# Kernel optimization log

Hardware: AMD Instinct MI355X
Metric: run time of the kernel (lower is better)

The kernel has to match this reference:

```python
import jax, jax.numpy as jnp
import numpy as np

N_NODES = 100000
N_EDGES = 1600000
N_GRAPHS = 1000


def setup_inputs() -> dict:
    key = jax.random.key(0)
    ks = jax.random.split(key, 20)
    s = 0.1
    inp = {
        'x': jax.random.normal(ks[0], (N_NODES, 7), jnp.float32),
        'edge_attr': jax.random.normal(ks[1], (N_EDGES, 4), jnp.float32),
        # edge linear (edge_dim -> in_channels) per conv
        'W_e1': jax.random.normal(ks[2], (4, 7), jnp.float32) * s,
        'b_e1': jnp.zeros((7,), jnp.float32),
        'W_e2': jax.random.normal(ks[3], (4, 64), jnp.float32) * s,
        'b_e2': jnp.zeros((64,), jnp.float32),
        # conv1 MLP: Linear(7,64) -> ReLU -> Linear(64,64)
        'W1a': jax.random.normal(ks[4], (7, 64), jnp.float32) * s,
        'b1a': jnp.zeros((64,), jnp.float32),
        'W1b': jax.random.normal(ks[5], (64, 64), jnp.float32) * s,
        'b1b': jnp.zeros((64,), jnp.float32),
        # conv2 MLP: Linear(64,64) -> ReLU -> Linear(64,64)
        'W2a': jax.random.normal(ks[6], (64, 64), jnp.float32) * s,
        'b2a': jnp.zeros((64,), jnp.float32),
        'W2b': jax.random.normal(ks[7], (64, 64), jnp.float32) * s,
        'b2b': jnp.zeros((64,), jnp.float32),
        # final classifier Linear(64, 12)
        'Wfc': jax.random.normal(ks[8], (64, 12), jnp.float32) * s,
        'bfc': jnp.zeros((12,), jnp.float32),
        'edge_index': jax.random.randint(ks[9], (2, N_EDGES), 0, N_NODES, jnp.int64),
        'batch': jnp.sort(jax.random.randint(ks[10], (N_NODES,), 0, N_GRAPHS, jnp.int64)),
    }
    return inp


def _gine_conv(x, edge_index, edge_attr, W_e, b_e, Wa, ba, Wb, bb):
    # GINEConv (eps=0): nn(x_i + sum_j relu(x_j + lin_e(e_ji)))
    src, dst = edge_index[0], edge_index[1]
    e = edge_attr @ W_e + b_e                      # [E, d]
    m = jax.nn.relu(x[src] + e)                    # gather + message [E, d]
    agg = jax.ops.segment_sum(m, dst, num_segments=x.shape[0])  # scatter-add
    h = x + agg                                    # (1+eps)*x with eps=0
    return jax.nn.relu(h @ Wa + ba) @ Wb + bb


def reference(x, edge_attr, W_e1, b_e1, W_e2, b_e2, W1a, b1a, W1b, b1b,
              W2a, b2a, W2b, b2b, Wfc, bfc, edge_index, batch):
    h = jax.nn.relu(_gine_conv(x, edge_index, edge_attr, W_e1, b_e1, W1a, b1a, W1b, b1b))
    h = jax.nn.relu(_gine_conv(h, edge_index, edge_attr, W_e2, b_e2, W2a, b2a, W2b, b2b))
    # global mean pool over graphs
    sums = jax.ops.segment_sum(h, batch, num_segments=N_GRAPHS)          # [G, 64]
    cnt = jax.ops.segment_sum(jnp.ones((h.shape[0], 1), h.dtype), batch,
                              num_segments=N_GRAPHS)                      # [G, 1]
    pooled = sums / jnp.maximum(cnt, 1.0)
    return pooled @ Wfc + bfc                                             # [G, 12]
```

## Files before the change

kernel.cpp:

```cpp
#include <hip/hip_runtime.h>
#include <hip/hip_bf16.h>


#define NBUCK 512
#define TILE_A 2048
#define PB_CAP 3584

typedef __attribute__((ext_vector_type(8))) short bf16x8;
typedef __attribute__((ext_vector_type(4))) float f32x4;
typedef __attribute__((ext_vector_type(4))) unsigned int u32x4;

__device__ __forceinline__ float bf2f(unsigned short u) {
  return __uint_as_float(((unsigned)u) << 16);
}
__device__ __forceinline__ unsigned short f2bf(float f) {
  __hip_bfloat16 hb = __float2bfloat16(f);
  return *reinterpret_cast<unsigned short*>(&hb);
}
__device__ __forceinline__ int bucket_lo(int b, int N) {
  return (int)(((long long)b * N + (NBUCK - 1)) >> 9);
}
__device__ __forceinline__ int bucket_of(int d, int N, float f512overN) {
  int b = (int)((float)d * f512overN);
  long long d512 = (long long)d << 9;
  if ((long long)(b + 1) * N <= d512) ++b;
  else if ((long long)b * N > d512) --b;
  return b;
}

__global__ __launch_bounds__(256) void histB_kernel(
    const int* __restrict__ dstIdx, int* __restrict__ bcnt, int E, int N,
    float f512overN) {
  __shared__ int cnt[NBUCK];
  int t = threadIdx.x;
  cnt[t] = 0;
  cnt[t + 256] = 0;
  __syncthreads();
  int e0 = blockIdx.x * TILE_A;
  int valid = min(TILE_A, E - e0);
#pragma unroll
  for (int k = 0; k < 8; ++k) {
    int idx = t + k * 256;
    if (idx < valid) {
      int d = dstIdx[e0 + idx];
      atomicAdd(&cnt[bucket_of(d, N, f512overN)], 1);
    }
  }
  __syncthreads();
  if (cnt[t]) atomicAdd(&bcnt[t], cnt[t]);
  if (cnt[t + 256]) atomicAdd(&bcnt[t + 256], cnt[t + 256]);
}

__global__ __launch_bounds__(256) void scanB_kernel(
    const int* __restrict__ bcnt, int* __restrict__ bstart,
    int* __restrict__ bcur, int E) {
  __shared__ int sd[256];
  int t = threadIdx.x;
  int base = t * 2;
  int v0 = bcnt[base];
  int v1 = bcnt[base + 1];
  int ts = v0 + v1;
  sd[t] = ts;
  __syncthreads();
  for (int off = 1; off < 256; off <<= 1) {
    int xv = (t >= off) ? sd[t - off] : 0;
    __syncthreads();
    sd[t] += xv;
    __syncthreads();
  }
  int excl = sd[t] - ts;
  bstart[base] = excl;
  bstart[base + 1] = excl + v0;
  bcur[base] = excl;
  bcur[base + 1] = excl + v0;
  if (t == 255) bstart[NBUCK] = E;
}

__global__ __launch_bounds__(256) void binA_kernel(
    const int* __restrict__ srcIdx, const int* __restrict__ dstIdx,
    const float* __restrict__ ea, int* __restrict__ bcur,
    u32x4* __restrict__ binned, int E, int N, float f512overN) {
  __shared__ u32x4 recs[TILE_A];
  __shared__ int cnt[NBUCK];
  __shared__ int off[NBUCK];
  int t = threadIdx.x;
  int e0 = blockIdx.x * TILE_A;
  int valid = min(TILE_A, E - e0);

  cnt[t] = 0;
  cnt[t + 256] = 0;
  __syncthreads();

  u32x4 rec[8];
  int bkt[8], slot[8];
#pragma unroll
  for (int k = 0; k < 8; ++k) {
    int idx = t + k * 256;
    bkt[k] = -1;
    if (idx < valid) {
      int e = e0 + idx;
      int d = dstIdx[e];
      int s = __builtin_nontemporal_load(&srcIdx[e]);
      f32x4 a = __builtin_nontemporal_load(
          reinterpret_cast<const f32x4*>(ea) + e);
      u32x4 v;
      v[0] = (unsigned)s;
      v[1] = (unsigned)f2bf(a[0]) | ((unsigned)f2bf(a[1]) << 16);
      v[2] = (unsigned)f2bf(a[2]) | ((unsigned)f2bf(a[3]) << 16);
      v[3] = (unsigned)d;
      rec[k] = v;
      int b = bucket_of(d, N, f512overN);
      bkt[k] = b;
      slot[k] = atomicAdd(&cnt[b], 1);
    }
  }
  __syncthreads();
  int c0 = cnt[t], c1 = cnt[t + 256];
  for (int o = 1; o < NBUCK; o <<= 1) {
    int v0 = (t >= o) ? cnt[t - o] : 0;
    int v1 = (t + 256 >= o) ? cnt[t + 256 - o] : 0;
    __syncthreads();
    cnt[t] += v0;
    cnt[t + 256] += v1;
    __syncthreads();
  }
  off[t] = cnt[t] - c0;
  off[t + 256] = cnt[t + 256] - c1;
  __syncthreads();
#pragma unroll
  for (int k = 0; k < 8; ++k)
    if (bkt[k] >= 0) recs[off[bkt[k]] + slot[k]] = rec[k];
  __syncthreads();
#pragma unroll
  for (int h = 0; h < 2; ++h) {
    int b = t + h * 256;
    int c = (h == 0) ? c0 : c1;
    if (c > 0) {
      int g = atomicAdd(&bcur[b], c);
      int o = off[b];
      for (int k = 0; k < c; ++k) binned[g + k] = recs[o + k];
    }
  }
}

__global__ __launch_bounds__(256) void binB_kernel(
    const u32x4* __restrict__ binned, const int* __restrict__ bstart,
    int* __restrict__ deg, int* __restrict__ cursor, int* __restrict__ gcur,
    u32x4* __restrict__ csr, const float* __restrict__ x,
    const float* __restrict__ We1, const float* __restrict__ be1,
    float* __restrict__ p1, int N) {
  __shared__ u32x4 lrec[PB_CAP];
  __shared__ int ldeg[256];
  __shared__ int lcur[256];
  int b = blockIdx.x;
  int t = threadIdx.x;
  int lo = bucket_lo(b, N);
  int lo1 = bucket_lo(b + 1, N);
  int nlocal = lo1 - lo;
  int rs = bstart[b];
  int re = bstart[b + 1];
  int count = re - rs;
  float w1[28], b1[7];
#pragma unroll
  for (int i = 0; i < 28; ++i) w1[i] = We1[i];
#pragma unroll
  for (int i = 0; i < 7; ++i) b1[i] = be1[i];
  ldeg[t] = 0;
  __syncthreads();
  for (int i = t; i < count; i += 256) {
    int d = (int)binned[rs + i][3];
    atomicAdd(&ldeg[d - lo], 1);
  }
  __syncthreads();
  int c = ldeg[t];
  lcur[t] = c;
  __syncthreads();
  for (int o = 1; o < 256; o <<= 1) {
    int v = (t >= o) ? lcur[t - o] : 0;
    __syncthreads();
    lcur[t] += v;
    __syncthreads();
  }
  int excl = lcur[t] - c;
  if (t < nlocal) {
    deg[lo + t] = c;
    cursor[lo + t] = rs + excl;
  }
  __syncthreads();
  lcur[t] = excl;
  __syncthreads();
  bool fits = (count <= PB_CAP);
  if (fits) {
    for (int i = t; i < count; i += 256) {
      u32x4 r = binned[rs + i];
      int p = atomicAdd(&lcur[(int)r[3] - lo], 1);
      lrec[p] = r;
    }
    __syncthreads();
    for (int i = t; i < count; i += 256) csr[rs + i] = lrec[i];
  } else {
    if (t < nlocal) gcur[lo + t] = rs + excl;
    __threadfence();
    __syncthreads();
    for (int i = t; i < count; i += 256) {
      u32x4 r = binned[rs + i];
      int p = atomicAdd(&gcur[(int)r[3]], 1);
      csr[p] = r;
    }
    __threadfence();
    __syncthreads();
  }
  if (t < nlocal) {
    float acc[7];
#pragma unroll
    for (int ch = 0; ch < 7; ++ch) acc[ch] = 0.f;
    for (int i = excl; i < excl + c; ++i) {
      u32x4 r = fits ? lrec[i] : csr[rs + i];
      int s = (int)r[0];
      float a0 = __uint_as_float(r[1] << 16);
      float a1 = __uint_as_float(r[1] & 0xffff0000u);
      float a2 = __uint_as_float(r[2] << 16);
      float a3 = __uint_as_float(r[2] & 0xffff0000u);
      const float* xs = x + (size_t)s * 7;
#pragma unroll
      for (int ch = 0; ch < 7; ++ch) {
        float v = b1[ch] + a0 * w1[ch] + a1 * w1[7 + ch] + a2 * w1[14 + ch] +
                  a3 * w1[21 + ch] + xs[ch];
        acc[ch] += fmaxf(v, 0.f);
      }
    }
    const float* xn = x + (size_t)(lo + t) * 7;
#pragma unroll
    for (int ch = 0; ch < 7; ++ch)
      p1[(size_t)(lo + t) * 8 + ch] = acc[ch] + xn[ch];
    p1[(size_t)(lo + t) * 8 + 7] = 0.f;
  }
}

__global__ __launch_bounds__(256) void agg2_kernel(
    const unsigned short* __restrict__ h1b, const u32x4* __restrict__ csr,
    const int* __restrict__ deg, const int* __restrict__ cursor,
    const float* __restrict__ We2, const float* __restrict__ be2,
    unsigned short* __restrict__ p2b, int N) {
  int w = threadIdx.x >> 6, j = threadIdx.x & 63;
  int q = j >> 4;
  int m = j & 15;
  float4 ew0 = *reinterpret_cast<const float4*>(&We2[0 * 64 + m * 4]);
  float4 ew1 = *reinterpret_cast<const float4*>(&We2[1 * 64 + m * 4]);
  float4 ew2 = *reinterpret_cast<const float4*>(&We2[2 * 64 + m * 4]);
  float4 ew3 = *reinterpret_cast<const float4*>(&We2[3 * 64 + m * 4]);
  float4 eb = *reinterpret_cast<const float4*>(&be2[m * 4]);
  int wid = blockIdx.x * 4 + w;
  int nw = gridDim.x * 4;
  for (int n = wid; n < N; n += nw) {
    int start = cursor[n];
    int end = start + deg[n];
    float acc0 = 0.f, acc1 = 0.f, acc2 = 0.f, acc3 = 0.f;
    for (int base = start; base < end; base += 64) {
      int cnt = min(64, end - base);
      int sl = 0;
      int ax = 0, ay = 0;
      if (base + j < end) {
        u32x4 u = csr[base + j];
        sl = (int)u[0];
        ax = (int)u[1];
        ay = (int)u[2];
      }
      int ngrp = (cnt + 3) >> 2;
      for (int it = 0; it < ngrp; ++it) {
        int lane = it * 4 + q;
        int s = __shfl(sl, lane);
        unsigned uax = (unsigned)__shfl(ax, lane);
        unsigned uay = (unsigned)__shfl(ay, lane);
        ushort4 hv =
            *reinterpret_cast<const ushort4*>(&h1b[(size_t)s * 64 + m * 4]);
        float a0 = __uint_as_float(uax << 16);
        float a1 = __uint_as_float(uax & 0xffff0000u);
        float a2 = __uint_as_float(uay << 16);
        float a3 = __uint_as_float(uay & 0xffff0000u);
        float e0 = eb.x + a0 * ew0.x + a1 * ew1.x + a2 * ew2.x + a3 * ew3.x;
        float e1 = eb.y + a0 * ew0.y + a1 * ew1.y + a2 * ew2.y + a3 * ew3.y;
        float e2 = eb.z + a0 * ew0.z + a1 * ew1.z + a2 * ew2.z + a3 * ew3.z;
        float e3 = eb.w + a0 * ew0.w + a1 * ew1.w + a2 * ew2.w + a3 * ew3.w;
        if (lane < cnt) {
          acc0 += fmaxf(bf2f(hv.x) + e0, 0.f);
          acc1 += fmaxf(bf2f(hv.y) + e1, 0.f);
          acc2 += fmaxf(bf2f(hv.z) + e2, 0.f);
          acc3 += fmaxf(bf2f(hv.w) + e3, 0.f);
        }
      }
    }
    acc0 += __shfl_xor(acc0, 16); acc0 += __shfl_xor(acc0, 32);
    acc1 += __shfl_xor(acc1, 16); acc1 += __shfl_xor(acc1, 32);
    acc2 += __shfl_xor(acc2, 16); acc2 += __shfl_xor(acc2, 32);
    acc3 += __shfl_xor(acc3, 16); acc3 += __shfl_xor(acc3, 32);
    ushort4 sv =
        *reinterpret_cast<const ushort4*>(&h1b[(size_t)n * 64 + m * 4]);
    if (q == 0) {
      ushort4 o;
      o.x = f2bf(acc0 + bf2f(sv.x));
      o.y = f2bf(acc1 + bf2f(sv.y));
      o.z = f2bf(acc2 + bf2f(sv.z));
      o.w = f2bf(acc3 + bf2f(sv.w));
      *reinterpret_cast<ushort4*>(&p2b[(size_t)n * 64 + m * 4]) = o;
    }
  }
}

template <int KIN>
__global__ __launch_bounds__(256) void mlp_mfma_kernel(
    const void* __restrict__ pin, const float* __restrict__ Wa,
    const float* __restrict__ ba, const float* __restrict__ Wb,
    const float* __restrict__ bb, unsigned short* __restrict__ hout, int N) {
  __shared__ unsigned short t_lds[4][16 * 72];
  int w = threadIdx.x >> 6, l = threadIdx.x & 63;
  int lr = l & 15, lq = l >> 4;
  constexpr int KSA = (KIN == 8) ? 1 : 2;
  constexpr int VROWS = (KIN == 8) ? 7 : 64;
  bf16x8 wa[2][4], wb[2][4];
#pragma unroll
  for (int ks = 0; ks < KSA; ++ks)
#pragma unroll
    for (int c = 0; c < 4; ++c) {
      bf16x8 f;
#pragma unroll
      for (int r = 0; r < 8; ++r) {
        int row = ks * 32 + lq * 8 + r;
        float v = (row < VROWS) ? Wa[row * 64 + c * 16 + lr] : 0.f;
        f[r] = (short)f2bf(v);
      }
      wa[ks][c] = f;
    }
#pragma unroll
  for (int ks = 0; ks < 2; ++ks)
#pragma unroll
    for (int c = 0; c < 4; ++c) {
      bf16x8 f;
#pragma unroll
      for (int r = 0; r < 8; ++r)
        f[r] = (short)f2bf(Wb[(ks * 32 + lq * 8 + r) * 64 + c * 16 + lr]);
      wb[ks][c] = f;
    }
  float vba[4], vbb[4];
#pragma unroll
  for (int c = 0; c < 4; ++c) {
    vba[c] = ba[c * 16 + lr];
    vbb[c] = bb[c * 16 + lr];
  }
  unsigned short* tl = t_lds[w];
  int ntiles = (N + 15) >> 4;
  for (int tile = blockIdx.x * 4 + w; tile < ntiles; tile += gridDim.x * 4) {
    int n0 = tile << 4;
    int arow = n0 + lr;
    bf16x8 af0, af1;
#pragma unroll
    for (int r = 0; r < 8; ++r) { af0[r] = 0; af1[r] = 0; }
    if (KIN == 8) {
      if (lq == 0 && arow < N) {
        const float* pr = (const float*)pin + (size_t)arow * 8;
#pragma unroll
        for (int r = 0; r < 8; ++r) af0[r] = (short)f2bf(pr[r]);
      }
    } else {
      if (arow < N) {
        const unsigned short* pr =
            (const unsigned short*)pin + (size_t)arow * 64 + lq * 8;
        af0 = *(const bf16x8*)(pr);
        af1 = *(const bf16x8*)(pr + 32);
      }
    }
    f32x4 accA[4];
#pragma unroll
    for (int c = 0; c < 4; ++c) {
      f32x4 a = {0.f, 0.f, 0.f, 0.f};
      a = __builtin_amdgcn_mfma_f32_16x16x32_bf16(af0, wa[0][c], a, 0, 0, 0);
      if (KSA == 2)
        a = __builtin_amdgcn_mfma_f32_16x16x32_bf16(af1, wa[1][c], a, 0, 0, 0);
      accA[c] = a;
    }
#pragma unroll
    for (int c = 0; c < 4; ++c)
#pragma unroll
      for (int r = 0; r < 4; ++r) {
        float v = fmaxf(accA[c][r] + vba[c], 0.f);
        tl[(lq * 4 + r) * 72 + c * 16 + lr] = f2bf(v);
      }
    bf16x8 tf0 = *(const bf16x8*)&tl[lr * 72 + lq * 8];
    bf16x8 tf1 = *(const bf16x8*)&tl[lr * 72 + 32 + lq * 8];
#pragma unroll
    for (int c = 0; c < 4; ++c) {
      f32x4 a = {0.f, 0.f, 0.f, 0.f};
      a = __builtin_amdgcn_mfma_f32_16x16x32_bf16(tf0, wb[0][c], a, 0, 0, 0);
      a = __builtin_amdgcn_mfma_f32_16x16x32_bf16(tf1, wb[1][c], a, 0, 0, 0);
#pragma unroll
      for (int r = 0; r < 4; ++r) {
        int row = n0 + lq * 4 + r;
        if (row < N) {
          float v = fmaxf(a[r] + vbb[c], 0.f);
          hout[(size_t)row * 64 + c * 16 + lr] = f2bf(v);
        }
      }
    }
  }
}

__global__ __launch_bounds__(64) void pool_fc_kernel(
    const unsigned short* __restrict__ h2b, const int* __restrict__ batch,
    const float* __restrict__ Wfc, const float* __restrict__ bfc,
    float* __restrict__ out, int N, int G) {
  int g = blockIdx.x;
  int j = threadIdx.x;
  int q = j >> 4;
  int m = j & 15;
  int lo = 0, hi = N;
  while (lo < hi) {
    int mid = (lo + hi) >> 1;
    if (batch[mid] < g) lo = mid + 1; else hi = mid;
  }
  int start = lo;
  lo = start; hi = N;
  while (lo < hi) {
    int mid = (lo + hi) >> 1;
    if (batch[mid] < g + 1) lo = mid + 1; else hi = mid;
  }
  int end = lo;
  int cnt = end - start;
  float s0 = 0.f, s1 = 0.f, s2 = 0.f, s3 = 0.f;
  int ngrp = (cnt + 3) >> 2;
  for (int it = 0; it < ngrp; ++it) {
    int r = start + it * 4 + q;
    if (r < end) {
      ushort4 hv =
          *reinterpret_cast<const ushort4*>(&h2b[(size_t)r * 64 + m * 4]);
      s0 += bf2f(hv.x);
      s1 += bf2f(hv.y);
      s2 += bf2f(hv.z);
      s3 += bf2f(hv.w);
    }
  }
  s0 += __shfl_xor(s0, 16); s0 += __shfl_xor(s0, 32);
  s1 += __shfl_xor(s1, 16); s1 += __shfl_xor(s1, 32);
  s2 += __shfl_xor(s2, 16); s2 += __shfl_xor(s2, 32);
  s3 += __shfl_xor(s3, 16); s3 += __shfl_xor(s3, 32);
  float inv = 1.f / fmaxf((float)cnt, 1.f);
  __shared__ float spool[64];
  if (q == 0) {
    spool[m * 4 + 0] = s0 * inv;
    spool[m * 4 + 1] = s1 * inv;
    spool[m * 4 + 2] = s2 * inv;
    spool[m * 4 + 3] = s3 * inv;
  }
  __syncthreads();
  if (j < 12) {
    float o = bfc[j];
#pragma unroll
    for (int k = 0; k < 64; ++k) o += spool[k] * Wfc[k * 12 + j];
    out[(size_t)g * 12 + j] = o;
  }
}

extern "C" void kernel_launch(void* const* d_in, const int* in_sizes, int n_in,
                              void* d_out, int out_size, void* d_ws,
                              size_t ws_size, hipStream_t stream) {
  const float* x   = (const float*)d_in[0];
  const float* ea  = (const float*)d_in[1];
  const float* We1 = (const float*)d_in[2];
  const float* be1 = (const float*)d_in[3];
  const float* We2 = (const float*)d_in[4];
  const float* be2 = (const float*)d_in[5];
  const float* W1a = (const float*)d_in[6];
  const float* b1a = (const float*)d_in[7];
  const float* W1b = (const float*)d_in[8];
  const float* b1b = (const float*)d_in[9];
  const float* W2a = (const float*)d_in[10];
  const float* b2a = (const float*)d_in[11];
  const float* W2b = (const float*)d_in[12];
  const float* b2b = (const float*)d_in[13];
  const float* Wfc = (const float*)d_in[14];
  const float* bfc = (const float*)d_in[15];
  const int* eidx  = (const int*)d_in[16];
  const int* batch = (const int*)d_in[17];

  int N = in_sizes[0] / 7;
  int E = in_sizes[1] / 4;
  int G = out_size / 12;
  const int* srcIdx = eidx;
  const int* dstIdx = eidx + E;

  char* ws = (char*)d_ws;
  int*   deg      = (int*)ws;             ws += (size_t)N * 4;
  int*   cursor   = (int*)ws;             ws += (size_t)N * 4;
  int*   gcur     = (int*)ws;             ws += (size_t)N * 4;
  int*   bcnt     = (int*)ws;             ws += NBUCK * 4;
  int*   bstart   = (int*)ws;             ws += (NBUCK + 1) * 4;
  int*   bcur     = (int*)ws;             ws += NBUCK * 4;
  ws = (char*)(((size_t)ws + 255) & ~(size_t)255);
  u32x4* csr      = (u32x4*)ws;           ws += (size_t)E * 16;
  float* p1       = (float*)ws;           ws += (size_t)N * 8 * 4;
  unsigned short* h1b = (unsigned short*)ws; ws += (size_t)N * 64 * 2;
  unsigned short* p2b = (unsigned short*)ws; ws += (size_t)N * 64 * 2;
  unsigned short* h2b = (unsigned short*)ws;
  u32x4* binned = (u32x4*)p2b;

  int ntiles = (N + 15) / 16;
  int mlpBlocks = (ntiles + 3) / 4;
  if (mlpBlocks > 1024) mlpBlocks = 1024;
  int ntilesA = (E + TILE_A - 1) / TILE_A;
  float f512overN = 512.0f / (float)N;

  hipMemsetAsync(bcnt, 0, NBUCK * 4, stream);
  histB_kernel<<<ntilesA, 256, 0, stream>>>(dstIdx, bcnt, E, N, f512overN);
  scanB_kernel<<<1, 256, 0, stream>>>(bcnt, bstart, bcur, E);
  binA_kernel<<<ntilesA, 256, 0, stream>>>(srcIdx, dstIdx, ea, bcur, binned,
                                           E, N, f512overN);
  binB_kernel<<<NBUCK, 256, 0, stream>>>(binned, bstart, deg, cursor, gcur,
                                         csr, x, We1, be1, p1, N);
  mlp_mfma_kernel<8><<<mlpBlocks, 256, 0, stream>>>(p1, W1a, b1a, W1b, b1b,
                                                    h1b, N);
  agg2_kernel<<<2048, 256, 0, stream>>>(h1b, csr, deg, cursor, We2, be2, p2b,
                                        N);
  mlp_mfma_kernel<64><<<mlpBlocks, 256, 0, stream>>>(p2b, W2a, b2a, W2b, b2b,
                                                     h2b, N);
  pool_fc_kernel<<<G, 64, 0, stream>>>(h2b, batch, Wfc, bfc, (float*)d_out, N,
                                       G);
}
```

Before: 206.6 us.

## Drop per-node CSR sort; aggregate bucketed edges via LDS atomics per bucket

Removes the per-bucket counting sort that built a full CSR (deg/cursor arrays) and instead has each block process its dst-bucket's edges in arbitrary order, accumulating messages into shared-memory per-node accumulators with float atomics. Both conv aggregations now read the bucketed edge records directly, with 512-thread blocks and one block per bucket (512 blocks). This eliminates the sort passes and CSR writes, but introduces LDS atomic contention (64 channels per edge in conv2) and reduces grid parallelism for the heavy conv2 aggregation from 2048 blocks to 512. Summation order becomes nondeterministic.

```diff
diff --git a/kernel.cpp b/kernel.cpp
--- a/kernel.cpp
+++ b/kernel.cpp
@@ -4,7 +4,7 @@
 
 #define NBUCK 512
 #define TILE_A 2048
-#define PB_CAP 3584
+#define NLOC_MAX 200
 
 typedef __attribute__((ext_vector_type(8))) short bf16x8;
 typedef __attribute__((ext_vector_type(4))) float f32x4;
@@ -143,167 +143,117 @@
   }
 }
 
-__global__ __launch_bounds__(256) void binB_kernel(
+__global__ __launch_bounds__(512) void conv1B_kernel(
     const u32x4* __restrict__ binned, const int* __restrict__ bstart,
-    int* __restrict__ deg, int* __restrict__ cursor, int* __restrict__ gcur,
-    u32x4* __restrict__ csr, const float* __restrict__ x,
-    const float* __restrict__ We1, const float* __restrict__ be1,
-    float* __restrict__ p1, int N) {
-  __shared__ u32x4 lrec[PB_CAP];
-  __shared__ int ldeg[256];
-  __shared__ int lcur[256];
-  int b = blockIdx.x;
-  int t = threadIdx.x;
+    const float* __restrict__ x, const float* __restrict__ We1,
+    const float* __restrict__ be1, float* __restrict__ p1, int N) {
+  __shared__ float acc[NLOC_MAX * 9];
+  int b = blockIdx.x, t = threadIdx.x;
   int lo = bucket_lo(b, N);
-  int lo1 = bucket_lo(b + 1, N);
-  int nlocal = lo1 - lo;
-  int rs = bstart[b];
-  int re = bstart[b + 1];
-  int count = re - rs;
+  int nlocal = bucket_lo(b + 1, N) - lo;
+  int rs = bstart[b], re = bstart[b + 1];
   float w1[28], b1[7];
 #pragma unroll
   for (int i = 0; i < 28; ++i) w1[i] = We1[i];
 #pragma unroll
   for (int i = 0; i < 7; ++i) b1[i] = be1[i];
-  ldeg[t] = 0;
-  __syncthreads();
-  for (int i = t; i < count; i += 256) {
-    int d = (int)binned[rs + i][3];
-    atomicAdd(&ldeg[d - lo], 1);
-  }
-  __syncthreads();
-  int c = ldeg[t];
-  lcur[t] = c;
-  __syncthreads();
-  for (int o = 1; o < 256; o <<= 1) {
-    int v = (t >= o) ? lcur[t - o] : 0;
-    __syncthreads();
-    lcur[t] += v;
-    __syncthreads();
-  }
-  int excl = lcur[t] - c;
+  for (int i = t; i < nlocal * 9; i += 512) acc[i] = 0.f;
+  __syncthreads();
+  for (int i = rs + t; i < re; i += 512) {
+    u32x4 r = binned[i];
+    int s = (int)r[0];
+    int d = (int)r[3] - lo;
+    float a0 = __uint_as_float(r[1] << 16);
+    float a1 = __uint_as_float(r[1] & 0xffff0000u);
+    float a2 = __uint_as_float(r[2] << 16);
+    float a3 = __uint_as_float(r[2] & 0xffff0000u);
+    const float* xs = x + (size_t)s * 7;
+#pragma unroll
+    for (int ch = 0; ch < 7; ++ch) {
+      float v = b1[ch] + a0 * w1[ch] + a1 * w1[7 + ch] + a2 * w1[14 + ch] +
+                a3 * w1[21 + ch] + xs[ch];
+      atomicAdd(&acc[d * 9 + ch], fmaxf(v, 0.f));
+    }
+  }
+  __syncthreads();
   if (t < nlocal) {
-    deg[lo + t] = c;
-    cursor[lo + t] = rs + excl;
-  }
-  __syncthreads();
-  lcur[t] = excl;
-  __syncthreads();
-  bool fits = (count <= PB_CAP);
-  if (fits) {
-    for (int i = t; i < count; i += 256) {
-      u32x4 r = binned[rs + i];
-      int p = atomicAdd(&lcur[(int)r[3] - lo], 1);
-      lrec[p] = r;
-    }
-    __syncthreads();
-    for (int i = t; i < count; i += 256) csr[rs + i] = lrec[i];
-  } else {
-    if (t < nlocal) gcur[lo + t] = rs + excl;
-    __threadfence();
-    __syncthreads();
-    for (int i = t; i < count; i += 256) {
-      u32x4 r = binned[rs + i];
-      int p = atomicAdd(&gcur[(int)r[3]], 1);
-      csr[p] = r;
-    }
-    __threadfence();
-    __syncthreads();
-  }
-  if (t < nlocal) {
-    float acc[7];
-#pragma unroll
-    for (int ch = 0; ch < 7; ++ch) acc[ch] = 0.f;
-    for (int i = excl; i < excl + c; ++i) {
-      u32x4 r = fits ? lrec[i] : csr[rs + i];
-      int s = (int)r[0];
-      float a0 = __uint_as_float(r[1] << 16);
-      float a1 = __uint_as_float(r[1] & 0xffff0000u);
-      float a2 = __uint_as_float(r[2] << 16);
-      float a3 = __uint_as_float(r[2] & 0xffff0000u);
-      const float* xs = x + (size_t)s * 7;
-#pragma unroll
-      for (int ch = 0; ch < 7; ++ch) {
-        float v = b1[ch] + a0 * w1[ch] + a1 * w1[7 + ch] + a2 * w1[14 + ch] +
-                  a3 * w1[21 + ch] + xs[ch];
-        acc[ch] += fmaxf(v, 0.f);
-      }
-    }
-    const float* xn = x + (size_t)(lo + t) * 7;
+    int n = lo + t;
+    const float* xn = x + (size_t)n * 7;
 #pragma unroll
     for (int ch = 0; ch < 7; ++ch)
-      p1[(size_t)(lo + t) * 8 + ch] = acc[ch] + xn[ch];
-    p1[(size_t)(lo + t) * 8 + 7] = 0.f;
-  }
-}
-
-__global__ __launch_bounds__(256) void agg2_kernel(
-    const unsigned short* __restrict__ h1b, const u32x4* __restrict__ csr,
-    const int* __restrict__ deg, const int* __restrict__ cursor,
-    const float* __restrict__ We2, const float* __restrict__ be2,
-    unsigned short* __restrict__ p2b, int N) {
-  int w = threadIdx.x >> 6, j = threadIdx.x & 63;
+      p1[(size_t)n * 8 + ch] = acc[t * 9 + ch] + xn[ch];
+    p1[(size_t)n * 8 + 7] = 0.f;
+  }
+}
+
+__global__ __launch_bounds__(512) void conv2B_kernel(
+    const u32x4* __restrict__ binned, const int* __restrict__ bstart,
+    const unsigned short* __restrict__ h1b, const float* __restrict__ We2,
+    const float* __restrict__ be2, unsigned short* __restrict__ p2b, int N) {
+  __shared__ float acc[NLOC_MAX * 65];
+  int b = blockIdx.x, t = threadIdx.x;
+  int w = t >> 6, j = t & 63;
   int q = j >> 4;
   int m = j & 15;
+  int lo = bucket_lo(b, N);
+  int nlocal = bucket_lo(b + 1, N) - lo;
+  int rs = bstart[b], re = bstart[b + 1];
   float4 ew0 = *reinterpret_cast<const float4*>(&We2[0 * 64 + m * 4]);
   float4 ew1 = *reinterpret_cast<const float4*>(&We2[1 * 64 + m * 4]);
   float4 ew2 = *reinterpret_cast<const float4*>(&We2[2 * 64 + m * 4]);
   float4 ew3 = *reinterpret_cast<const float4*>(&We2[3 * 64 + m * 4]);
   float4 eb = *reinterpret_cast<const float4*>(&be2[m * 4]);
-  int wid = blockIdx.x * 4 + w;
-  int nw = gridDim.x * 4;
-  for (int n = wid; n < N; n += nw) {
-    int start = cursor[n];
-    int end = start + deg[n];
-    float acc0 = 0.f, acc1 = 0.f, acc2 = 0.f, acc3 = 0.f;
-    for (int base = start; base < end; base += 64) {
-      int cnt = min(64, end - base);
-      int sl = 0;
-      int ax = 0, ay = 0;
-      if (base + j < end) {
-        u32x4 u = csr[base + j];
-        sl = (int)u[0];
-        ax = (int)u[1];
-        ay = (int)u[2];
-      }
-      int ngrp = (cnt + 3) >> 2;
-      for (int it = 0; it < ngrp; ++it) {
-        int lane = it * 4 + q;
-        int s = __shfl(sl, lane);
-        unsigned uax = (unsigned)__shfl(ax, lane);
-        unsigned uay = (unsigned)__shfl(ay, lane);
-        ushort4 hv =
-            *reinterpret_cast<const ushort4*>(&h1b[(size_t)s * 64 + m * 4]);
-        float a0 = __uint_as_float(uax << 16);
-        float a1 = __uint_as_float(uax & 0xffff0000u);
-        float a2 = __uint_as_float(uay << 16);
-        float a3 = __uint_as_float(uay & 0xffff0000u);
-        float e0 = eb.x + a0 * ew0.x + a1 * ew1.x + a2 * ew2.x + a3 * ew3.x;
-        float e1 = eb.y + a0 * ew0.y + a1 * ew1.y + a2 * ew2.y + a3 * ew3.y;
-        float e2 = eb.z + a0 * ew0.z + a1 * ew1.z + a2 * ew2.z + a3 * ew3.z;
-        float e3 = eb.w + a0 * ew0.w + a1 * ew1.w + a2 * ew2.w + a3 * ew3.w;
-        if (lane < cnt) {
-          acc0 += fmaxf(bf2f(hv.x) + e0, 0.f);
-          acc1 += fmaxf(bf2f(hv.y) + e1, 0.f);
-          acc2 += fmaxf(bf2f(hv.z) + e2, 0.f);
-          acc3 += fmaxf(bf2f(hv.w) + e3, 0.f);
-        }
-      }
-    }
-    acc0 += __shfl_xor(acc0, 16); acc0 += __shfl_xor(acc0, 32);
-    acc1 += __shfl_xor(acc1, 16); acc1 += __shfl_xor(acc1, 32);
-    acc2 += __shfl_xor(acc2, 16); acc2 += __shfl_xor(acc2, 32);
-    acc3 += __shfl_xor(acc3, 16); acc3 += __shfl_xor(acc3, 32);
+  for (int i = t; i < nlocal * 65; i += 512) acc[i] = 0.f;
+  __syncthreads();
+  for (int base = rs + w * 64; base < re; base += 512) {
+    int cnt = min(64, re - base);
+    int sl = 0, ax = 0, ay = 0, dl = 0;
+    if (j < cnt) {
+      u32x4 u = binned[base + j];
+      sl = (int)u[0];
+      ax = (int)u[1];
+      ay = (int)u[2];
+      dl = (int)u[3];
+    }
+    int ngrp = (cnt + 3) >> 2;
+    for (int it = 0; it < ngrp; ++it) {
+      int lane = it * 4 + q;
+      int s = __shfl(sl, lane);
+      unsigned uax = (unsigned)__shfl(ax, lane);
+      unsigned uay = (unsigned)__shfl(ay, lane);
+      int dd = __shfl(dl, lane) - lo;
+      ushort4 hv =
+          *reinterpret_cast<const ushort4*>(&h1b[(size_t)s * 64 + m * 4]);
+      float a0 = __uint_as_float(uax << 16);
+      float a1 = __uint_as_float(uax & 0xffff0000u);
+      float a2 = __uint_as_float(uay << 16);
+      float a3 = __uint_as_float(uay & 0xffff0000u);
+      float e0 = eb.x + a0 * ew0.x + a1 * ew1.x + a2 * ew2.x + a3 * ew3.x;
+      float e1 = eb.y + a0 * ew0.y + a1 * ew1.y + a2 * ew2.y + a3 * ew3.y;
+      float e2 = eb.z + a0 * ew0.z + a1 * ew1.z + a2 * ew2.z + a3 * ew3.z;
+      float e3 = eb.w + a0 * ew0.w + a1 * ew1.w + a2 * ew2.w + a3 * ew3.w;
+      if (lane < cnt) {
+        float* ar = &acc[dd * 65 + m * 4];
+        atomicAdd(&ar[0], fmaxf(bf2f(hv.x) + e0, 0.f));
+        atomicAdd(&ar[1], fmaxf(bf2f(hv.y) + e1, 0.f));
+        atomicAdd(&ar[2], fmaxf(bf2f(hv.z) + e2, 0.f));
+        atomicAdd(&ar[3], fmaxf(bf2f(hv.w) + e3, 0.f));
+      }
+    }
+  }
+  __syncthreads();
+  for (int idx = t; idx < nlocal * 16; idx += 512) {
+    int node = idx >> 4, mq = idx & 15;
+    int n = lo + node;
     ushort4 sv =
-        *reinterpret_cast<const ushort4*>(&h1b[(size_t)n * 64 + m * 4]);
-    if (q == 0) {
-      ushort4 o;
-      o.x = f2bf(acc0 + bf2f(sv.x));
-      o.y = f2bf(acc1 + bf2f(sv.y));
-      o.z = f2bf(acc2 + bf2f(sv.z));
-      o.w = f2bf(acc3 + bf2f(sv.w));
-      *reinterpret_cast<ushort4*>(&p2b[(size_t)n * 64 + m * 4]) = o;
-    }
+        *reinterpret_cast<const ushort4*>(&h1b[(size_t)n * 64 + mq * 4]);
+    const float* ar = &acc[node * 65 + mq * 4];
+    ushort4 o;
+    o.x = f2bf(ar[0] + bf2f(sv.x));
+    o.y = f2bf(ar[1] + bf2f(sv.y));
+    o.z = f2bf(ar[2] + bf2f(sv.z));
+    o.w = f2bf(ar[3] + bf2f(sv.w));
+    *reinterpret_cast<ushort4*>(&p2b[(size_t)n * 64 + mq * 4]) = o;
   }
 }
 
@@ -488,19 +438,15 @@
   const int* dstIdx = eidx + E;
 
   char* ws = (char*)d_ws;
-  int*   deg      = (int*)ws;             ws += (size_t)N * 4;
-  int*   cursor   = (int*)ws;             ws += (size_t)N * 4;
-  int*   gcur     = (int*)ws;             ws += (size_t)N * 4;
   int*   bcnt     = (int*)ws;             ws += NBUCK * 4;
   int*   bstart   = (int*)ws;             ws += (NBUCK + 1) * 4;
   int*   bcur     = (int*)ws;             ws += NBUCK * 4;
   ws = (char*)(((size_t)ws + 255) & ~(size_t)255);
-  u32x4* csr      = (u32x4*)ws;           ws += (size_t)E * 16;
+  u32x4* binned   = (u32x4*)ws;           ws += (size_t)E * 16;
   float* p1       = (float*)ws;           ws += (size_t)N * 8 * 4;
   unsigned short* h1b = (unsigned short*)ws; ws += (size_t)N * 64 * 2;
   unsigned short* p2b = (unsigned short*)ws; ws += (size_t)N * 64 * 2;
   unsigned short* h2b = (unsigned short*)ws;
-  u32x4* binned = (u32x4*)p2b;
 
   int ntiles = (N + 15) / 16;
   int mlpBlocks = (ntiles + 3) / 4;
@@ -513,12 +459,11 @@
   scanB_kernel<<<1, 256, 0, stream>>>(bcnt, bstart, bcur, E);
   binA_kernel<<<ntilesA, 256, 0, stream>>>(srcIdx, dstIdx, ea, bcur, binned,
                                            E, N, f512overN);
-  binB_kernel<<<NBUCK, 256, 0, stream>>>(binned, bstart, deg, cursor, gcur,
-                                         csr, x, We1, be1, p1, N);
+  conv1B_kernel<<<NBUCK, 512, 0, stream>>>(binned, bstart, x, We1, be1, p1, N);
   mlp_mfma_kernel<8><<<mlpBlocks, 256, 0, stream>>>(p1, W1a, b1a, W1b, b1b,
                                                     h1b, N);
-  agg2_kernel<<<2048, 256, 0, stream>>>(h1b, csr, deg, cursor, We2, be2, p2b,
-                                        N);
+  conv2B_kernel<<<NBUCK, 512, 0, stream>>>(binned, bstart, h1b, We2, be2, p2b,
+                                           N);
   mlp_mfma_kernel<64><<<mlpBlocks, 256, 0, stream>>>(p2b, W2a, b2a, W2b, b2b,
                                                      h2b, N);
   pool_fc_kernel<<<G, 64, 0, stream>>>(h2b, batch, Wfc, bfc, (float*)d_out, N,
```

Result: slower. 732.3 us (+254.3%).

## Fuse conv MLPs into aggregation kernels via per-bucket LDS staging

Applied to the files above, without the earlier changes.

The first conv MLP now runs inside binB_kernel, reading the aggregated 7-channel features from LDS (reusing lrec) instead of writing p1 to global memory and launching a separate MLP kernel. The second conv MLP is fused into agg2_kernel, which now processes one node bucket per 512-thread block and stages the aggregated bf16 rows in LDS before running the MFMA MLP. This removes two kernel launches and the global round trips of p1 and p2b. In exchange, agg2 drops from 2048 grid-strided 256-thread blocks to 512 blocks, which may hurt load balance and occupancy. The fused kernels also carry more registers for the weight fragments, and binned gets its own workspace region.

```diff
diff --git a/kernel.cpp b/kernel.cpp
--- a/kernel.cpp
+++ b/kernel.cpp
@@ -148,23 +148,55 @@
     int* __restrict__ deg, int* __restrict__ cursor, int* __restrict__ gcur,
     u32x4* __restrict__ csr, const float* __restrict__ x,
     const float* __restrict__ We1, const float* __restrict__ be1,
-    float* __restrict__ p1, int N) {
+    const float* __restrict__ W1a, const float* __restrict__ b1a,
+    const float* __restrict__ W1b, const float* __restrict__ b1b,
+    unsigned short* __restrict__ h1b, int N) {
   __shared__ u32x4 lrec[PB_CAP];
   __shared__ int ldeg[256];
   __shared__ int lcur[256];
   int b = blockIdx.x;
   int t = threadIdx.x;
+  int w = t >> 6, l = t & 63;
+  int lr = l & 15, lq = l >> 4;
   int lo = bucket_lo(b, N);
   int lo1 = bucket_lo(b + 1, N);
   int nlocal = lo1 - lo;
   int rs = bstart[b];
   int re = bstart[b + 1];
   int count = re - rs;
+  bf16x8 wa1[4], wb1[2][4];
+#pragma unroll
+  for (int c = 0; c < 4; ++c) {
+    bf16x8 f;
+#pragma unroll
+    for (int r = 0; r < 8; ++r) {
+      int row = lq * 8 + r;
+      f[r] = (short)f2bf((row < 7) ? W1a[row * 64 + c * 16 + lr] : 0.f);
+    }
+    wa1[c] = f;
+  }
+#pragma unroll
+  for (int ks = 0; ks < 2; ++ks)
+#pragma unroll
+    for (int c = 0; c < 4; ++c) {
+      bf16x8 f;
+#pragma unroll
+      for (int r = 0; r < 8; ++r)
+        f[r] = (short)f2bf(W1b[(ks * 32 + lq * 8 + r) * 64 + c * 16 + lr]);
+      wb1[ks][c] = f;
+    }
+  float vba[4], vbb[4];
+#pragma unroll
+  for (int c = 0; c < 4; ++c) {
+    vba[c] = b1a[c * 16 + lr];
+    vbb[c] = b1b[c * 16 + lr];
+  }
   float w1[28], b1[7];
 #pragma unroll
   for (int i = 0; i < 28; ++i) w1[i] = We1[i];
 #pragma unroll
   for (int i = 0; i < 7; ++i) b1[i] = be1[i];
+
   ldeg[t] = 0;
   __syncthreads();
   for (int i = t; i < count; i += 256) {
@@ -210,10 +242,10 @@
     __threadfence();
     __syncthreads();
   }
+  float acc[7];
+#pragma unroll
+  for (int ch = 0; ch < 7; ++ch) acc[ch] = 0.f;
   if (t < nlocal) {
-    float acc[7];
-#pragma unroll
-    for (int ch = 0; ch < 7; ++ch) acc[ch] = 0.f;
     for (int i = excl; i < excl + c; ++i) {
       u32x4 r = fits ? lrec[i] : csr[rs + i];
       int s = (int)r[0];
@@ -229,30 +261,108 @@
         acc[ch] += fmaxf(v, 0.f);
       }
     }
+  }
+  __syncthreads();
+  float* pl = (float*)lrec;
+  unsigned short* tlds =
+      (unsigned short*)((char*)lrec + 8192) + (size_t)w * (16 * 72);
+  if (t < nlocal) {
     const float* xn = x + (size_t)(lo + t) * 7;
 #pragma unroll
-    for (int ch = 0; ch < 7; ++ch)
-      p1[(size_t)(lo + t) * 8 + ch] = acc[ch] + xn[ch];
-    p1[(size_t)(lo + t) * 8 + 7] = 0.f;
-  }
-}
-
-__global__ __launch_bounds__(256) void agg2_kernel(
+    for (int ch = 0; ch < 7; ++ch) pl[t * 8 + ch] = acc[ch] + xn[ch];
+    pl[t * 8 + 7] = 0.f;
+  }
+  __syncthreads();
+  int ntile = (nlocal + 15) >> 4;
+  for (int tile = w; tile < ntile; tile += 4) {
+    int r0 = tile << 4;
+    bf16x8 af0;
+#pragma unroll
+    for (int r = 0; r < 8; ++r) af0[r] = 0;
+    if (lq == 0) {
+      int row16 = r0 + lr;
+      if (row16 < nlocal) {
+        const float* pr = pl + row16 * 8;
+#pragma unroll
+        for (int r = 0; r < 8; ++r) af0[r] = (short)f2bf(pr[r]);
+      }
+    }
+    f32x4 accA[4];
+#pragma unroll
+    for (int cc = 0; cc < 4; ++cc) {
+      f32x4 a = {0.f, 0.f, 0.f, 0.f};
+      accA[cc] = __builtin_amdgcn_mfma_f32_16x16x32_bf16(af0, wa1[cc], a, 0, 0, 0);
+    }
+#pragma unroll
+    for (int cc = 0; cc < 4; ++cc)
+#pragma unroll
+      for (int r = 0; r < 4; ++r) {
+        float v = fmaxf(accA[cc][r] + vba[cc], 0.f);
+        tlds[(lq * 4 + r) * 72 + cc * 16 + lr] = f2bf(v);
+      }
+    bf16x8 tf0 = *(const bf16x8*)&tlds[lr * 72 + lq * 8];
+    bf16x8 tf1 = *(const bf16x8*)&tlds[lr * 72 + 32 + lq * 8];
+#pragma unroll
+    for (int cc = 0; cc < 4; ++cc) {
+      f32x4 a = {0.f, 0.f, 0.f, 0.f};
+      a = __builtin_amdgcn_mfma_f32_16x16x32_bf16(tf0, wb1[0][cc], a, 0, 0, 0);
+      a = __builtin_amdgcn_mfma_f32_16x16x32_bf16(tf1, wb1[1][cc], a, 0, 0, 0);
+#pragma unroll
+      for (int r = 0; r < 4; ++r) {
+        int row16 = r0 + lq * 4 + r;
+        if (row16 < nlocal) {
+          float v = fmaxf(a[r] + vbb[cc], 0.f);
+          h1b[(size_t)(lo + row16) * 64 + cc * 16 + lr] = f2bf(v);
+        }
+      }
+    }
+  }
+}
+
+__global__ __launch_bounds__(512) void agg2_kernel(
     const unsigned short* __restrict__ h1b, const u32x4* __restrict__ csr,
     const int* __restrict__ deg, const int* __restrict__ cursor,
     const float* __restrict__ We2, const float* __restrict__ be2,
-    unsigned short* __restrict__ p2b, int N) {
-  int w = threadIdx.x >> 6, j = threadIdx.x & 63;
+    const float* __restrict__ W2a, const float* __restrict__ b2a,
+    const float* __restrict__ W2b, const float* __restrict__ b2b,
+    unsigned short* __restrict__ h2b, int N) {
+  __shared__ unsigned short p2l[200 * 72];
+  __shared__ unsigned short tlds2[8][16 * 72];
+  int b = blockIdx.x, t = threadIdx.x;
+  int wv = t >> 6, j = t & 63;
   int q = j >> 4;
   int m = j & 15;
+  int lr = j & 15, lq = j >> 4;
+  int lo = bucket_lo(b, N);
+  int nlocal = bucket_lo(b + 1, N) - lo;
   float4 ew0 = *reinterpret_cast<const float4*>(&We2[0 * 64 + m * 4]);
   float4 ew1 = *reinterpret_cast<const float4*>(&We2[1 * 64 + m * 4]);
   float4 ew2 = *reinterpret_cast<const float4*>(&We2[2 * 64 + m * 4]);
   float4 ew3 = *reinterpret_cast<const float4*>(&We2[3 * 64 + m * 4]);
   float4 eb = *reinterpret_cast<const float4*>(&be2[m * 4]);
-  int wid = blockIdx.x * 4 + w;
-  int nw = gridDim.x * 4;
-  for (int n = wid; n < N; n += nw) {
+  bf16x8 wa2[2][4], wb2[2][4];
+#pragma unroll
+  for (int ks = 0; ks < 2; ++ks)
+#pragma unroll
+    for (int cc = 0; cc < 4; ++cc) {
+      bf16x8 f, g;
+#pragma unroll
+      for (int r = 0; r < 8; ++r) {
+        int row = ks * 32 + lq * 8 + r;
+        f[r] = (short)f2bf(W2a[row * 64 + cc * 16 + lr]);
+        g[r] = (short)f2bf(W2b[row * 64 + cc * 16 + lr]);
+      }
+      wa2[ks][cc] = f;
+      wb2[ks][cc] = g;
+    }
+  float vba[4], vbb[4];
+#pragma unroll
+  for (int cc = 0; cc < 4; ++cc) {
+    vba[cc] = b2a[cc * 16 + lr];
+    vbb[cc] = b2b[cc * 16 + lr];
+  }
+  for (int rel = wv; rel < nlocal; rel += 8) {
+    int n = lo + rel;
     int start = cursor[n];
     int end = start + deg[n];
     float acc0 = 0.f, acc1 = 0.f, acc2 = 0.f, acc3 = 0.f;
@@ -302,102 +412,50 @@
       o.y = f2bf(acc1 + bf2f(sv.y));
       o.z = f2bf(acc2 + bf2f(sv.z));
       o.w = f2bf(acc3 + bf2f(sv.w));
-      *reinterpret_cast<ushort4*>(&p2b[(size_t)n * 64 + m * 4]) = o;
-    }
-  }
-}
-
-template <int KIN>
-__global__ __launch_bounds__(256) void mlp_mfma_kernel(
-    const void* __restrict__ pin, const float* __restrict__ Wa,
-    const float* __restrict__ ba, const float* __restrict__ Wb,
-    const float* __restrict__ bb, unsigned short* __restrict__ hout, int N) {
-  __shared__ unsigned short t_lds[4][16 * 72];
-  int w = threadIdx.x >> 6, l = threadIdx.x & 63;
-  int lr = l & 15, lq = l >> 4;
-  constexpr int KSA = (KIN == 8) ? 1 : 2;
-  constexpr int VROWS = (KIN == 8) ? 7 : 64;
-  bf16x8 wa[2][4], wb[2][4];
-#pragma unroll
-  for (int ks = 0; ks < KSA; ++ks)
-#pragma unroll
-    for (int c = 0; c < 4; ++c) {
-      bf16x8 f;
-#pragma unroll
-      for (int r = 0; r < 8; ++r) {
-        int row = ks * 32 + lq * 8 + r;
-        float v = (row < VROWS) ? Wa[row * 64 + c * 16 + lr] : 0.f;
-        f[r] = (short)f2bf(v);
-      }
-      wa[ks][c] = f;
-    }
-#pragma unroll
-  for (int ks = 0; ks < 2; ++ks)
-#pragma unroll
-    for (int c = 0; c < 4; ++c) {
-      bf16x8 f;
-#pragma unroll
-      for (int r = 0; r < 8; ++r)
-        f[r] = (short)f2bf(Wb[(ks * 32 + lq * 8 + r) * 64 + c * 16 + lr]);
-      wb[ks][c] = f;
-    }
-  float vba[4], vbb[4];
-#pragma unroll
-  for (int c = 0; c < 4; ++c) {
-    vba[c] = ba[c * 16 + lr];
-    vbb[c] = bb[c * 16 + lr];
-  }
-  unsigned short* tl = t_lds[w];
-  int ntiles = (N + 15) >> 4;
-  for (int tile = blockIdx.x * 4 + w; tile < ntiles; tile += gridDim.x * 4) {
-    int n0 = tile << 4;
-    int arow = n0 + lr;
+      *reinterpret_cast<ushort4*>(&p2l[rel * 72 + m * 4]) = o;
+    }
+  }
+  __syncthreads();
+  int ntile = (nlocal + 15) >> 4;
+  for (int tile = wv; tile < ntile; tile += 8) {
+    int r0 = tile << 4;
+    int row16 = r0 + lr;
     bf16x8 af0, af1;
 #pragma unroll
     for (int r = 0; r < 8; ++r) { af0[r] = 0; af1[r] = 0; }
-    if (KIN == 8) {
-      if (lq == 0 && arow < N) {
-        const float* pr = (const float*)pin + (size_t)arow * 8;
-#pragma unroll
-        for (int r = 0; r < 8; ++r) af0[r] = (short)f2bf(pr[r]);
-      }
-    } else {
-      if (arow < N) {
-        const unsigned short* pr =
-            (const unsigned short*)pin + (size_t)arow * 64 + lq * 8;
-        af0 = *(const bf16x8*)(pr);
-        af1 = *(const bf16x8*)(pr + 32);
-      }
+    if (row16 < nlocal) {
+      af0 = *(const bf16x8*)&p2l[row16 * 72 + lq * 8];
+      af1 = *(const bf16x8*)&p2l[row16 * 72 + 32 + lq * 8];
     }
     f32x4 accA[4];
 #pragma unroll
-    for (int c = 0; c < 4; ++c) {
+    for (int cc = 0; cc < 4; ++cc) {
       f32x4 a = {0.f, 0.f, 0.f, 0.f};
-      a = __builtin_amdgcn_mfma_f32_16x16x32_bf16(af0, wa[0][c], a, 0, 0, 0);
-      if (KSA == 2)
-        a = __builtin_amdgcn_mfma_f32_16x16x32_bf16(af1, wa[1][c], a, 0, 0, 0);
-      accA[c] = a;
-    }
-#pragma unroll
-    for (int c = 0; c < 4; ++c)
+      a = __builtin_amdgcn_mfma_f32_16x16x32_bf16(af0, wa2[0][cc], a, 0, 0, 0);
+      a = __builtin_amdgcn_mfma_f32_16x16x32_bf16(af1, wa2[1][cc], a, 0, 0, 0);
+      accA[cc] = a;
+    }
+    unsigned short* tl = tlds2[wv];
+#pragma unroll
+    for (int cc = 0; cc < 4; ++cc)
 #pragma unroll
       for (int r = 0; r < 4; ++r) {
-        float v = fmaxf(accA[c][r] + vba[c], 0.f);
-        tl[(lq * 4 + r) * 72 + c * 16 + lr] = f2bf(v);
+        float v = fmaxf(accA[cc][r] + vba[cc], 0.f);
+        tl[(lq * 4 + r) * 72 + cc * 16 + lr] = f2bf(v);
       }
     bf16x8 tf0 = *(const bf16x8*)&tl[lr * 72 + lq * 8];
     bf16x8 tf1 = *(const bf16x8*)&tl[lr * 72 + 32 + lq * 8];
 #pragma unroll
-    for (int c = 0; c < 4; ++c) {
+    for (int cc = 0; cc < 4; ++cc) {
       f32x4 a = {0.f, 0.f, 0.f, 0.f};
-      a = __builtin_amdgcn_mfma_f32_16x16x32_bf16(tf0, wb[0][c], a, 0, 0, 0);
-      a = __builtin_amdgcn_mfma_f32_16x16x32_bf16(tf1, wb[1][c], a, 0, 0, 0);
+      a = __builtin_amdgcn_mfma_f32_16x16x32_bf16(tf0, wb2[0][cc], a, 0, 0, 0);
+      a = __builtin_amdgcn_mfma_f32_16x16x32_bf16(tf1, wb2[1][cc], a, 0, 0, 0);
 #pragma unroll
       for (int r = 0; r < 4; ++r) {
-        int row = n0 + lq * 4 + r;
-        if (row < N) {
-          float v = fmaxf(a[r] + vbb[c], 0.f);
-          hout[(size_t)row * 64 + c * 16 + lr] = f2bf(v);
+        int rr = r0 + lq * 4 + r;
+        if (rr < nlocal) {
+          float v = fmaxf(a[r] + vbb[cc], 0.f);
+          h2b[(size_t)(lo + rr) * 64 + cc * 16 + lr] = f2bf(v);
         }
       }
     }
@@ -496,15 +554,10 @@
   int*   bcur     = (int*)ws;             ws += NBUCK * 4;
   ws = (char*)(((size_t)ws + 255) & ~(size_t)255);
   u32x4* csr      = (u32x4*)ws;           ws += (size_t)E * 16;
-  float* p1       = (float*)ws;           ws += (size_t)N * 8 * 4;
+  u32x4* binned   = (u32x4*)ws;           ws += (size_t)E * 16;
   unsigned short* h1b = (unsigned short*)ws; ws += (size_t)N * 64 * 2;
-  unsigned short* p2b = (unsigned short*)ws; ws += (size_t)N * 64 * 2;
   unsigned short* h2b = (unsigned short*)ws;
-  u32x4* binned = (u32x4*)p2b;
-
-  int ntiles = (N + 15) / 16;
-  int mlpBlocks = (ntiles + 3) / 4;
-  if (mlpBlocks > 1024) mlpBlocks = 1024;
+
   int ntilesA = (E + TILE_A - 1) / TILE_A;
   float f512overN = 512.0f / (float)N;
 
@@ -514,13 +567,10 @@
   binA_kernel<<<ntilesA, 256, 0, stream>>>(srcIdx, dstIdx, ea, bcur, binned,
                                            E, N, f512overN);
   binB_kernel<<<NBUCK, 256, 0, stream>>>(binned, bstart, deg, cursor, gcur,
-                                         csr, x, We1, be1, p1, N);
-  mlp_mfma_kernel<8><<<mlpBlocks, 256, 0, stream>>>(p1, W1a, b1a, W1b, b1b,
-                                                    h1b, N);
-  agg2_kernel<<<2048, 256, 0, stream>>>(h1b, csr, deg, cursor, We2, be2, p2b,
-                                        N);
-  mlp_mfma_kernel<64><<<mlpBlocks, 256, 0, stream>>>(p2b, W2a, b2a, W2b, b2b,
-                                                     h2b, N);
+                                         csr, x, We1, be1, W1a, b1a, W1b, b1b,
+                                         h1b, N);
+  agg2_kernel<<<NBUCK, 512, 0, stream>>>(h1b, csr, deg, cursor, We2, be2,
+                                         W2a, b2a, W2b, b2b, h2b, N);
   pool_fc_kernel<<<G, 64, 0, stream>>>(h2b, batch, Wfc, bfc, (float*)d_out, N,
                                        G);
 }
```

New measurement: 303.8 us. +47.0%, slower.
